# Performance work log

Hardware: AMD Instinct MI355X
Metric: run time of the kernel (lower is better)

Reference implementation:

```python
import jax, jax.numpy as jnp
import numpy as np

K = 10      # neighbors; conv width math 10 -> 3 -> 1
EPS = 1e-5  # InstanceNorm2d default eps (affine=False)
NEG = 0.2   # leaky relu slope


def _instnorm(x):
    m = x.mean(axis=(2, 3), keepdims=True)
    v = x.var(axis=(2, 3), keepdims=True)  # biased var, as in torch instance_norm
    return (x - m) * jax.lax.rsqrt(v + EPS)


def _conv13(x, w, b, s):
    y = jax.lax.conv_general_dilated(x, w, (1, s), 'VALID',
                                     dimension_numbers=('NCHW', 'OIHW', 'NCHW'))
    return y + b[None, :, None, None]


def _block(x, wA, bA, wB, bB):
    # Sequential(conv(1,3,stride(1,3)), IN, ReLU, conv(1,3), IN, ReLU)
    y = jax.nn.relu(_instnorm(_conv13(x, wA, bA, 3)))
    return jax.nn.relu(_instnorm(_conv13(y, wB, bB, 1)))


def _knn_idx(coords, k):
    # coords [B,2,N] -> k nearest neighbor indices [B,N,k] (self excluded)
    pts = coords.transpose(0, 2, 1)
    sq = (pts ** 2).sum(-1)
    dist = sq[:, :, None] + sq[:, None, :] - 2.0 * jnp.einsum('bnc,bmc->bnm', pts, pts)
    dist = jnp.clip(dist, 1e-12)
    _, idx = jax.lax.top_k(-dist, k + 1)  # smallest distances, sorted
    return idx[:, :, 1:]


def _gather_nb(x, idx):
    # x [B,C,N], idx [B,N,k] -> [B,C,N,k]
    return jax.vmap(lambda f, i: f[:, i])(x, idx)


def _graph_feat(feats, idx):
    nb = _gather_nb(feats, idx)
    ctr = jnp.broadcast_to(feats[..., None], nb.shape)
    return jnp.concatenate([ctr, nb - ctr], axis=1)  # [B,2C,N,k]


def _cos_angle(coords, idx):
    nei = _gather_nb(coords, idx)          # [B,2,N,k]
    ctr = coords[..., None]                # [B,2,N,1]
    dot = (ctr * nei).sum(axis=1, keepdims=True)
    na = jnp.sqrt((ctr ** 2).sum(axis=1, keepdims=True))
    nb = jnp.sqrt((nei ** 2).sum(axis=1, keepdims=True))
    return dot / (na * nb)                 # [B,1,N,k]


def _c1(w, x):
    # 1x1 conv, no bias
    return jnp.einsum('oi,bihw->bohw', w, x)


def _forward(coords, features, W1, W2, W3, W3o, a1wA, a1bA, a1wB, a1bB,
             a2wA, a2bA, a2wB, a2bB, angwA, angbA, angwB, angbB):
    B, C, N = features.shape
    lrelu = lambda x: jax.nn.leaky_relu(x, NEG)
    x0 = features[..., None]
    # KNN depends only on coords: all three torch graph builds give identical indices
    idx = _knn_idx(coords, K)
    x1_old = _graph_feat(features, idx)                         # [B,2C,N,K]
    x1 = _block(x1_old, a1wA, a1bA, a1wB, a1bB)                 # [B,C,N,1]
    # angle_enc1 is shared and idx identical -> f_ang1 == f_ang2
    f_ang = _block(_cos_angle(coords, idx), angwA, angbA, angwB, angbB)
    x2 = _block(_graph_feat(x1[..., 0], idx), a2wA, a2bA, a2wB, a2bB)
    x3 = jnp.concatenate([x0, x1 + f_ang, x2 + f_ang], axis=1)  # [B,3C,N,1]
    x3 = lrelu(_instnorm(_c1(W3, x3))).reshape(B, -1, N)
    x1o = lrelu(_instnorm(_c1(W1, x1_old))).max(axis=-1, keepdims=True)   # [B,C,N,1]
    x2o = lrelu(_instnorm(_c1(W2, _graph_feat(x1o[..., 0], idx)))).max(axis=-1, keepdims=True)
    x3o = jnp.concatenate([x0, x1o, x2o], axis=1)               # [B,4C,N,1]
    x3o = lrelu(_instnorm(_c1(W3o, x3o))).reshape(B, -1, N)
    return x3 + x3o


def setup_inputs():
    key = jax.random.key(0)
    ks = jax.random.split(key, 20)
    B, C, N = 4, 128, 4096
    r = lambda i, shp, sc=1.0: jax.random.normal(ks[i], shp, jnp.float32) * sc
    s = 0.05
    return {
        'coords': r(0, (B, 2, N)),
        'features': r(1, (B, C, N)),
        'W1': r(2, (C, 2 * C), s),
        'W2': r(3, (2 * C, 2 * C), s),
        'W3': r(4, (C, 3 * C), s),
        'W3o': r(5, (C, 4 * C), s),
        'a1wA': r(6, (C, 2 * C, 1, 3), s), 'a1bA': r(7, (C,), s),
        'a1wB': r(8, (C, C, 1, 3), s), 'a1bB': r(9, (C,), s),
        'a2wA': r(10, (C, 2 * C, 1, 3), s), 'a2bA': r(11, (C,), s),
        'a2wB': r(12, (C, C, 1, 3), s), 'a2bB': r(13, (C,), s),
        'angwA': r(14, (C, 1, 1, 3), s), 'angbA': r(15, (C,), s),
        'angwB': r(16, (C, C, 1, 3), s), 'angbB': r(17, (C,), s),
    }


def reference(coords, features, W1, W2, W3, W3o, a1wA, a1bA, a1wB, a1bB,
              a2wA, a2bA, a2wB, a2bB, angwA, angbA, angwB, angbB):
    return _forward(coords, features, W1, W2, W3, W3o, a1wA, a1bA, a1wB, a1bB,
                    a2wA, a2bA, a2wB, a2bB, angwA, angbA, angwB, angbB)
```

## Files before the change

### kernel.cpp

```cpp
#include <hip/hip_runtime.h>
#include <hip/hip_bf16.h>

typedef unsigned long long ull;

#define BN 4
#define CH 128
#define NP 4096
#define KNB 10
#define EPSI 1e-5f
#define GM_PTS 16
#define CA_PTS 8

__device__ __forceinline__ ull shfl_xor_u64(ull v, int mask) {
    unsigned lo = (unsigned)(v & 0xFFFFFFFFu);
    unsigned hi = (unsigned)(v >> 32);
    lo = __shfl_xor(lo, mask);
    hi = __shfl_xor(hi, mask);
    return ((ull)hi << 32) | lo;
}

__device__ __forceinline__ int clampj(int j) { return ((unsigned)j < (unsigned)NP) ? j : 0; }

__global__ void pack_convA(const float* __restrict__ w, float* __restrict__ WT) {
    int i = blockIdx.x * 256 + threadIdx.x;
    if (i >= 4 * CH * CH) return;
    int co = i % CH, ci = (i / CH) % CH, s = i / (CH * CH);
    float val;
    if (s == 0) {
        val = 0.f;
        for (int dk = 0; dk < 3; dk++)
            val += w[(co * 256 + ci) * 3 + dk] - w[(co * 256 + 128 + ci) * 3 + dk];
    } else {
        val = w[(co * 256 + 128 + ci) * 3 + (s - 1)];
    }
    WT[i] = val;
}

__global__ void pack_convB(const float* __restrict__ w, float* __restrict__ WT) {
    int i = blockIdx.x * 256 + threadIdx.x;
    if (i >= 3 * CH * CH) return;
    int co = i % CH, ci = (i / CH) % CH, dk = i / (CH * CH);
    WT[i] = w[(co * CH + ci) * 3 + dk];
}

__global__ void pack_uv(const float* __restrict__ w, float* __restrict__ WuT,
                        float* __restrict__ WnT, int Cout) {
    int i = blockIdx.x * 256 + threadIdx.x;
    if (i >= Cout * CH) return;
    int co = i % Cout, ci = i / Cout;
    float a = w[co * 256 + ci], b = w[co * 256 + 128 + ci];
    WuT[i] = a - b;
    WnT[i] = b;
}

__global__ void pack_plain(const float* __restrict__ w, float* __restrict__ WT, int Cin, int Cout) {
    int i = blockIdx.x * 256 + threadIdx.x;
    if (i >= Cin * Cout) return;
    int co = i % Cout, ci = i / Cout;
    WT[i] = w[co * Cin + ci];
}

__global__ void ftrans_kernel(const float* __restrict__ feats, float* __restrict__ F) {
    int i = blockIdx.x * 256 + threadIdx.x;
    if (i >= BN * CH * NP) return;
    int n = i % NP, c = (i / NP) % CH, b = i / (NP * CH);
    F[(b * NP + n) * CH + c] = feats[i];
}

__global__ void knn_kernel(const float* __restrict__ coords, int* __restrict__ IDX) {
    int gw = blockIdx.x * 4 + (threadIdx.x >> 6);
    int b = gw / NP;
    int n = gw % NP;
    int lane = threadIdx.x & 63;
    float xn = coords[(b * 2 + 0) * NP + n];
    float yn = coords[(b * 2 + 1) * NP + n];
    float sn = __fadd_rn(__fmul_rn(xn, xn), __fmul_rn(yn, yn));
    ull a[11];
    #pragma unroll
    for (int q = 0; q < 11; q++) a[q] = 0xFFFFFFFFFFFFFFFFULL;
    for (int m = lane; m < NP; m += 64) {
        float xm = coords[(b * 2 + 0) * NP + m];
        float ym = coords[(b * 2 + 1) * NP + m];
        float sm = __fadd_rn(__fmul_rn(xm, xm), __fmul_rn(ym, ym));
        float dot = __fmaf_rn(yn, ym, __fmul_rn(xn, xm));
        float d = __fsub_rn(__fadd_rn(sn, sm), __fmul_rn(2.0f, dot));
        d = fmaxf(d, 1e-12f);
        ull key = ((ull)__float_as_uint(d) << 32) | (unsigned)m;
        if (key < a[10]) {
            a[10] = key;
            #pragma unroll
            for (int q = 10; q > 0; --q)
                if (a[q] < a[q - 1]) { ull t = a[q]; a[q] = a[q - 1]; a[q - 1] = t; }
        }
    }
    int p = 0;
    for (int r = 0; r < 11; ++r) {
        ull k = (p < 11) ? a[p] : 0xFFFFFFFFFFFFFFFFULL;
        ull mk = k;
        #pragma unroll
        for (int off = 1; off < 64; off <<= 1) {
            ull o = shfl_xor_u64(mk, off);
            mk = (o < mk) ? o : mk;
        }
        if (k == mk) ++p;
        if (lane == 0 && r > 0) IDX[(b * NP + n) * KNB + (r - 1)] = (int)(mk & 0xFFFFFFFFu);
    }
}

__global__ void cosangle_kernel(const float* __restrict__ coords, const int* __restrict__ IDX,
                                float* __restrict__ COSA) {
    int i = blockIdx.x * 256 + threadIdx.x;
    if (i >= BN * NP * KNB) return;
    int n = (i / KNB) % NP, b = i / (KNB * NP);
    int j = clampj(IDX[i]);
    float xc = coords[(b * 2 + 0) * NP + n], yc = coords[(b * 2 + 1) * NP + n];
    float xm = coords[(b * 2 + 0) * NP + j], ym = coords[(b * 2 + 1) * NP + j];
    float dot = xc * xm + yc * ym;
    float na = sqrtf(xc * xc + yc * yc);
    float nb2 = sqrtf(xm * xm + ym * ym);
    COSA[i] = dot / fmaxf(na * nb2, 1e-30f);
}

__global__ __launch_bounds__(256) void convA_kernel(const float* __restrict__ Fin,
                             const int* __restrict__ IDX,
                             const float* __restrict__ WT, float* __restrict__ YA,
                             float* __restrict__ PART) {
    __shared__ float ctr[CA_PTS][CH];
    __shared__ float nb[CA_PTS][9][CH];
    __shared__ int jidx[CA_PTS * 9];
    int b = blockIdx.x / (NP / CA_PTS);
    int chunk = blockIdx.x % (NP / CA_PTS);
    int n0 = chunk * CA_PTS;
    int co = threadIdx.x & 127;
    int half = threadIdx.x >> 7;
    if (threadIdx.x < CA_PTS * 9) {
        int n = threadIdx.x / 9, kk = threadIdx.x % 9;
        jidx[threadIdx.x] = clampj(IDX[(b * NP + n0 + n) * KNB + kk]);
    }
    __syncthreads();
    for (int n = half; n < CA_PTS; n += 2)
        ctr[n][co] = Fin[(b * NP + n0 + n) * CH + co];
    for (int v = half; v < CA_PTS * 9; v += 2)
        nb[v / 9][v % 9][co] = Fin[(b * NP + jidx[v]) * CH + co];
    __syncthreads();
    const int nbase = half * 4;
    float cacc[4] = {0.f, 0.f, 0.f, 0.f};
    for (int ci = 0; ci < CH; ci++) {
        float w = WT[ci * CH + co];
        #pragma unroll
        for (int q = 0; q < 4; q++) cacc[q] += w * ctr[nbase + q][ci];
    }
    float acc[4][3];
    #pragma unroll
    for (int q = 0; q < 4; q++)
        #pragma unroll
        for (int t = 0; t < 3; t++) acc[q][t] = cacc[q];
    for (int dk = 0; dk < 3; dk++) {
        const float* Wd = WT + (1 + dk) * CH * CH;
        for (int ci = 0; ci < CH; ci++) {
            float w = Wd[ci * CH + co];
            #pragma unroll
            for (int q = 0; q < 4; q++)
                #pragma unroll
                for (int t = 0; t < 3; t++)
                    acc[q][t] += w * nb[nbase + q][t * 3 + dk][ci];
        }
    }
    float sum = 0.f, sq = 0.f;
    #pragma unroll
    for (int q = 0; q < 4; q++)
        #pragma unroll
        for (int t = 0; t < 3; t++) {
            float v = acc[q][t];
            YA[((b * NP + n0 + nbase + q) * 3 + t) * CH + co] = v;
            sum += v; sq += v * v;
        }
    int ch2 = chunk * 2 + half;
    PART[((b * (NP / CA_PTS * 2) + ch2) * 256 + co) * 2 + 0] = sum;
    PART[((b * (NP / CA_PTS * 2) + ch2) * 256 + co) * 2 + 1] = sq;
}

__global__ void angA_kernel(const float* __restrict__ COSA, const float* __restrict__ WT,
                            float* __restrict__ YA, float* __restrict__ PART) {
    __shared__ float ca[32][10];
    int b = blockIdx.x / (NP / 32);
    int chunk = blockIdx.x % (NP / 32);
    int n0 = chunk * 32;
    int co = threadIdx.x;
    for (int v = threadIdx.x; v < 320; v += 128) {
        int nn = v / 10, kk = v % 10;
        ca[nn][kk] = COSA[(b * NP + n0 + nn) * KNB + kk];
    }
    float w0 = WT[co], w1 = WT[CH + co], w2 = WT[2 * CH + co];
    __syncthreads();
    float sum = 0.f, sq = 0.f;
    for (int nn = 0; nn < 32; nn++) {
        #pragma unroll
        for (int t = 0; t < 3; t++) {
            float v = w0 * ca[nn][3 * t] + w1 * ca[nn][3 * t + 1] + w2 * ca[nn][3 * t + 2];
            YA[((b * NP + n0 + nn) * 3 + t) * CH + co] = v;
            sum += v; sq += v * v;
        }
    }
    PART[((b * (NP / 32) + chunk) * 256 + co) * 2 + 0] = sum;
    PART[((b * (NP / 32) + chunk) * 256 + co) * 2 + 1] = sq;
}

__global__ void pixel_gemm(const float* __restrict__ IN_, const float* __restrict__ WT,
                           float* __restrict__ OUT, int Cin, int Cout,
                           const float* __restrict__ STATS, int slot,
                           float* __restrict__ PART) {
    extern __shared__ float ldsin[];
    int b = blockIdx.x / (NP / 8);
    int chunk = blockIdx.x % (NP / 8);
    int n0 = chunk * 8;
    int co = threadIdx.x;
    if (slot >= 0) {
        for (int v = threadIdx.x; v < 8 * Cin; v += blockDim.x) {
            int c = v & 127;
            float m = STATS[((slot * BN + b) * 256 + c) * 2 + 0];
            float r = STATS[((slot * BN + b) * 256 + c) * 2 + 1];
            float x = (IN_[(size_t)(b * NP + n0) * Cin + v] - m) * r;
            ldsin[v] = fmaxf(x, 0.f);
        }
    } else {
        for (int v = threadIdx.x; v < 8 * Cin; v += blockDim.x)
            ldsin[v] = IN_[(size_t)(b * NP + n0) * Cin + v];
    }
    __syncthreads();
    float acc[8] = {0.f, 0.f, 0.f, 0.f, 0.f, 0.f, 0.f, 0.f};
    for (int ci = 0; ci < Cin; ci++) {
        float w = WT[ci * Cout + co];
        #pragma unroll
        for (int nn = 0; nn < 8; nn++) acc[nn] += w * ldsin[nn * Cin + ci];
    }
    float sum = 0.f, sq = 0.f;
    #pragma unroll
    for (int nn = 0; nn < 8; nn++) {
        OUT[(size_t)(b * NP + n0 + nn) * Cout + co] = acc[nn];
        sum += acc[nn]; sq += acc[nn] * acc[nn];
    }
    if (PART) {
        PART[((b * (NP / 8) + chunk) * 256 + co) * 2 + 0] = sum;
        PART[((b * (NP / 8) + chunk) * 256 + co) * 2 + 1] = sq;
    }
}

__global__ void stats_final(const float* __restrict__ PART, float* __restrict__ STATS,
                            int S, int Cc, int slot, int nch) {
    __shared__ float ssum[256], ssq[256];
    int bc = blockIdx.x;
    int b = bc / Cc, c = bc % Cc;
    float sum = 0.f, sq = 0.f;
    for (int ch = threadIdx.x; ch < nch; ch += 256) {
        sum += PART[((b * nch + ch) * 256 + c) * 2 + 0];
        sq  += PART[((b * nch + ch) * 256 + c) * 2 + 1];
    }
    ssum[threadIdx.x] = sum; ssq[threadIdx.x] = sq;
    __syncthreads();
    for (int s = 128; s > 0; s >>= 1) {
        if (threadIdx.x < s) {
            ssum[threadIdx.x] += ssum[threadIdx.x + s];
            ssq[threadIdx.x]  += ssq[threadIdx.x + s];
        }
        __syncthreads();
    }
    if (threadIdx.x == 0) {
        float mean = ssum[0] / (float)S;
        float var = fmaxf(ssq[0] / (float)S - mean * mean, 0.f);
        STATS[((slot * BN + b) * 256 + c) * 2 + 0] = mean;
        STATS[((slot * BN + b) * 256 + c) * 2 + 1] = rsqrtf(var + EPSI);
    }
}

__global__ void norm_act(float* __restrict__ X, const float* __restrict__ STATS,
                         int S, int Cc, int slot, int act) {
    int i = blockIdx.x * 256 + threadIdx.x;
    if (i >= BN * S * Cc) return;
    int c = i % Cc;
    int b = i / (S * Cc);
    float m = STATS[((slot * BN + b) * 256 + c) * 2 + 0];
    float r = STATS[((slot * BN + b) * 256 + c) * 2 + 1];
    float v = (X[i] - m) * r;
    if (act == 0) v = fmaxf(v, 0.f);
    else v = (v >= 0.f) ? v : 0.2f * v;
    X[i] = v;
}

__global__ void gathermax_fused(const float* __restrict__ X, const float* __restrict__ Wu,
                                const float* __restrict__ V, const int* __restrict__ IDX,
                                float* __restrict__ M, float* __restrict__ PART, int Cout) {
    __shared__ float rows[GM_PTS * CH];
    int b = blockIdx.x / (NP / GM_PTS);
    int chunk = blockIdx.x % (NP / GM_PTS);
    int n0 = chunk * GM_PTS;
    int c = threadIdx.x;
    for (int v = threadIdx.x; v < GM_PTS * CH; v += blockDim.x)
        rows[v] = X[(size_t)(b * NP + n0) * CH + v];
    __syncthreads();
    float acc[GM_PTS];
    #pragma unroll
    for (int nn = 0; nn < GM_PTS; nn++) acc[nn] = 0.f;
    for (int ci = 0; ci < CH; ci++) {
        float w = Wu[ci * Cout + c];
        #pragma unroll
        for (int nn = 0; nn < GM_PTS; nn++) acc[nn] += w * rows[nn * CH + ci];
    }
    float sum = 0.f, sq = 0.f;
    for (int nn = 0; nn < GM_PTS; nn++) {
        float u = acc[nn];
        float best = -3.4e38f;
        for (int k = 0; k < KNB; k++) {
            int j = clampj(IDX[(b * NP + n0 + nn) * KNB + k]);
            float v = u + V[(size_t)(b * NP + j) * Cout + c];
            sum += v; sq += v * v;
            best = fmaxf(best, v);
        }
        M[(size_t)(b * NP + n0 + nn) * Cout + c] = best;
    }
    PART[((b * (NP / GM_PTS) + chunk) * 256 + c) * 2 + 0] = sum;
    PART[((b * (NP / GM_PTS) + chunk) * 256 + c) * 2 + 1] = sq;
}

__global__ void head3_kernel(const float* __restrict__ F, const float* __restrict__ X1,
                             const float* __restrict__ X2, const float* __restrict__ FANG,
                             const float* __restrict__ WT, float* __restrict__ Y3,
                             float* __restrict__ PART) {
    __shared__ float lds[8 * 384];
    int b = blockIdx.x / (NP / 8);
    int chunk = blockIdx.x % (NP / 8);
    int n0 = chunk * 8;
    int co = threadIdx.x;
    for (int v = threadIdx.x; v < 8 * 384; v += 128) {
        int nn = v / 384, q = v % 384;
        int part = q / 128, ci = q % 128;
        size_t base = (size_t)(b * NP + n0 + nn) * CH + ci;
        float val;
        if (part == 0) val = F[base];
        else if (part == 1) val = X1[base] + FANG[base];
        else val = X2[base] + FANG[base];
        lds[v] = val;
    }
    __syncthreads();
    float acc[8] = {0.f, 0.f, 0.f, 0.f, 0.f, 0.f, 0.f, 0.f};
    for (int ci = 0; ci < 384; ci++) {
        float w = WT[ci * CH + co];
        #pragma unroll
        for (int nn = 0; nn < 8; nn++) acc[nn] += w * lds[nn * 384 + ci];
    }
    float sum = 0.f, sq = 0.f;
    #pragma unroll
    for (int nn = 0; nn < 8; nn++) {
        Y3[(size_t)(b * NP + n0 + nn) * CH + co] = acc[nn];
        sum += acc[nn]; sq += acc[nn] * acc[nn];
    }
    PART[((b * (NP / 8) + chunk) * 256 + co) * 2 + 0] = sum;
    PART[((b * (NP / 8) + chunk) * 256 + co) * 2 + 1] = sq;
}

__global__ void head3o_kernel(const float* __restrict__ F, const float* __restrict__ X1O,
                              const float* __restrict__ X2O, const float* __restrict__ WT,
                              float* __restrict__ Y3O, float* __restrict__ PART) {
    __shared__ float lds[8 * 512];
    int b = blockIdx.x / (NP / 8);
    int chunk = blockIdx.x % (NP / 8);
    int n0 = chunk * 8;
    int co = threadIdx.x;
    for (int v = threadIdx.x; v < 8 * 512; v += 128) {
        int nn = v / 512, q = v % 512;
        float val;
        if (q < 128) val = F[(size_t)(b * NP + n0 + nn) * CH + q];
        else if (q < 256) val = X1O[(size_t)(b * NP + n0 + nn) * CH + (q - 128)];
        else val = X2O[(size_t)(b * NP + n0 + nn) * 256 + (q - 256)];
        lds[v] = val;
    }
    __syncthreads();
    float acc[8] = {0.f, 0.f, 0.f, 0.f, 0.f, 0.f, 0.f, 0.f};
    for (int ci = 0; ci < 512; ci++) {
        float w = WT[ci * CH + co];
        #pragma unroll
        for (int nn = 0; nn < 8; nn++) acc[nn] += w * lds[nn * 512 + ci];
    }
    float sum = 0.f, sq = 0.f;
    #pragma unroll
    for (int nn = 0; nn < 8; nn++) {
        Y3O[(size_t)(b * NP + n0 + nn) * CH + co] = acc[nn];
        sum += acc[nn]; sq += acc[nn] * acc[nn];
    }
    PART[((b * (NP / 8) + chunk) * 256 + co) * 2 + 0] = sum;
    PART[((b * (NP / 8) + chunk) * 256 + co) * 2 + 1] = sq;
}

__global__ void final_kernel(const float* __restrict__ Y3, const float* __restrict__ Y3O,
                             const float* __restrict__ STATS, float* __restrict__ out) {
    __shared__ float T[64][129];
    int b = blockIdx.x / (NP / 64);
    int n0 = (blockIdx.x % (NP / 64)) * 64;
    int co = threadIdx.x;
    float m3 = STATS[((8 * BN + b) * 256 + co) * 2 + 0];
    float r3 = STATS[((8 * BN + b) * 256 + co) * 2 + 1];
    float m3o = STATS[((9 * BN + b) * 256 + co) * 2 + 0];
    float r3o = STATS[((9 * BN + b) * 256 + co) * 2 + 1];
    for (int j = 0; j < 64; j++) {
        size_t idx = (size_t)(b * NP + n0 + j) * CH + co;
        float v3 = (Y3[idx] - m3) * r3;
        v3 = (v3 >= 0.f) ? v3 : 0.2f * v3;
        float v3o = (Y3O[idx] - m3o) * r3o;
        v3o = (v3o >= 0.f) ? v3o : 0.2f * v3o;
        T[j][co] = v3 + v3o;
    }
    __syncthreads();
    for (int rr = 0; rr < 64; rr++) {
        int r = rr * 2 + (threadIdx.x >> 6);
        int j = threadIdx.x & 63;
        out[(size_t)(b * CH + r) * NP + n0 + j] = T[j][r];
    }
}

extern "C" void kernel_launch(void* const* d_in, const int* in_sizes, int n_in,
                              void* d_out, int out_size, void* d_ws, size_t ws_size,
                              hipStream_t stream) {
    const float* coords   = (const float*)d_in[0];
    const float* features = (const float*)d_in[1];
    const float* W1   = (const float*)d_in[2];
    const float* W2   = (const float*)d_in[3];
    const float* W3   = (const float*)d_in[4];
    const float* W3o  = (const float*)d_in[5];
    const float* a1wA = (const float*)d_in[6];
    const float* a1wB = (const float*)d_in[8];
    const float* a2wA = (const float*)d_in[10];
    const float* a2wB = (const float*)d_in[12];
    const float* angwA = (const float*)d_in[14];
    const float* angwB = (const float*)d_in[16];
    float* out = (float*)d_out;
    float* ws = (float*)d_ws;
    (void)ws_size; (void)in_sizes; (void)n_in; (void)out_size;

    size_t off = 0;
    float* WA1T  = ws + off; off += 4 * CH * CH;
    float* WA2T  = ws + off; off += 4 * CH * CH;
    float* WB1T  = ws + off; off += 3 * CH * CH;
    float* WB2T  = ws + off; off += 3 * CH * CH;
    float* WBAT  = ws + off; off += 3 * CH * CH;
    float* WANGA = ws + off; off += 512;
    float* W1U   = ws + off; off += CH * CH;
    float* W1N   = ws + off; off += CH * CH;
    float* W2U   = ws + off; off += CH * 256;
    float* W2N   = ws + off; off += CH * 256;
    float* W3T   = ws + off; off += 384 * CH;
    float* W3OT  = ws + off; off += 512 * CH;
    int*   IDX   = (int*)(ws + off); off += (size_t)BN * NP * KNB;
    float* COSA  = ws + off; off += (size_t)BN * NP * KNB;
    float* PART  = ws + off; off += (size_t)BN * 1024 * 256 * 2;
    float* STATS = ws + off; off += 10 * BN * 256 * 2;
    const size_t UNIT = (size_t)BN * NP * CH;
    float* POOL  = ws + off; off += 7 * UNIT;

    float* F    = POOL + 0 * UNIT;
    float* YA   = POOL + 1 * UNIT;
    float* X1   = POOL + 4 * UNIT;
    float* FANG = POOL + 5 * UNIT;
    float* X2   = POOL + 6 * UNIT;
    float* Y3   = POOL + 1 * UNIT;
    float* V1   = POOL + 2 * UNIT;
    float* M1   = POOL + 6 * UNIT;
    float* V2   = POOL + 4 * UNIT;
    float* M2   = POOL + 2 * UNIT;
    float* Y3O  = POOL + 4 * UNIT;

    pack_convA<<<(4 * CH * CH + 255) / 256, 256, 0, stream>>>(a1wA, WA1T);
    pack_convA<<<(4 * CH * CH + 255) / 256, 256, 0, stream>>>(a2wA, WA2T);
    pack_convB<<<(3 * CH * CH + 255) / 256, 256, 0, stream>>>(a1wB, WB1T);
    pack_convB<<<(3 * CH * CH + 255) / 256, 256, 0, stream>>>(a2wB, WB2T);
    pack_convB<<<(3 * CH * CH + 255) / 256, 256, 0, stream>>>(angwB, WBAT);
    pack_uv<<<(CH * CH + 255) / 256, 256, 0, stream>>>(W1, W1U, W1N, CH);
    pack_uv<<<(CH * 256 + 255) / 256, 256, 0, stream>>>(W2, W2U, W2N, 256);
    pack_plain<<<(384 * CH + 255) / 256, 256, 0, stream>>>(W3, W3T, 384, CH);
    pack_plain<<<(512 * CH + 255) / 256, 256, 0, stream>>>(W3o, W3OT, 512, CH);
    pack_plain<<<(3 * CH + 255) / 256, 256, 0, stream>>>(angwA, WANGA, 3, CH);

    ftrans_kernel<<<(BN * CH * NP + 255) / 256, 256, 0, stream>>>(features, F);
    knn_kernel<<<BN * NP / 4, 256, 0, stream>>>(coords, IDX);
    cosangle_kernel<<<(BN * NP * KNB + 255) / 256, 256, 0, stream>>>(coords, IDX, COSA);

    auto sfin = [&](int S, int Cc, int slot, int nch) {
        stats_final<<<BN * Cc, 256, 0, stream>>>(PART, STATS, S, Cc, slot, nch);
    };
    auto norm = [&](float* X, int S, int Cc, int slot, int act) {
        int tot = BN * S * Cc;
        norm_act<<<(tot + 255) / 256, 256, 0, stream>>>(X, STATS, S, Cc, slot, act);
    };

    convA_kernel<<<BN * (NP / CA_PTS), 256, 0, stream>>>(F, IDX, WA1T, YA, PART);
    sfin(3 * NP, CH, 0, NP / CA_PTS * 2);
    pixel_gemm<<<BN * (NP / 8), 128, 8 * 384 * 4, stream>>>(YA, WB1T, X1, 384, CH, STATS, 0, PART);
    sfin(NP, CH, 1, NP / 8);
    norm(X1, NP, CH, 1, 0);

    angA_kernel<<<BN * (NP / 32), 128, 0, stream>>>(COSA, WANGA, YA, PART);
    sfin(3 * NP, CH, 2, NP / 32);
    pixel_gemm<<<BN * (NP / 8), 128, 8 * 384 * 4, stream>>>(YA, WBAT, FANG, 384, CH, STATS, 2, PART);
    sfin(NP, CH, 3, NP / 8);
    norm(FANG, NP, CH, 3, 0);

    convA_kernel<<<BN * (NP / CA_PTS), 256, 0, stream>>>(X1, IDX, WA2T, YA, PART);
    sfin(3 * NP, CH, 4, NP / CA_PTS * 2);
    pixel_gemm<<<BN * (NP / 8), 128, 8 * 384 * 4, stream>>>(YA, WB2T, X2, 384, CH, STATS, 4, PART);
    sfin(NP, CH, 5, NP / 8);
    norm(X2, NP, CH, 5, 0);

    head3_kernel<<<BN * (NP / 8), 128, 0, stream>>>(F, X1, X2, FANG, W3T, Y3, PART);
    sfin(NP, CH, 8, NP / 8);

    pixel_gemm<<<BN * (NP / 8), 128, 8 * 128 * 4, stream>>>(F, W1N, V1, 128, CH, STATS, -1, nullptr);
    gathermax_fused<<<BN * (NP / GM_PTS), CH, 0, stream>>>(F, W1U, V1, IDX, M1, PART, CH);
    sfin(NP * KNB, CH, 6, NP / GM_PTS);
    norm(M1, NP, CH, 6, 1);

    pixel_gemm<<<BN * (NP / 8), 256, 8 * 128 * 4, stream>>>(M1, W2N, V2, 128, 256, STATS, -1, nullptr);
    gathermax_fused<<<BN * (NP / GM_PTS), 256, 0, stream>>>(M1, W2U, V2, IDX, M2, PART, 256);
    sfin(NP * KNB, 256, 7, NP / GM_PTS);
    norm(M2, NP, 256, 7, 1);

    head3o_kernel<<<BN * (NP / 8), 128, 0, stream>>>(F, M1, M2, W3OT, Y3O, PART);
    sfin(NP, CH, 9, NP / 8);
    final_kernel<<<BN * (NP / 64), 128, 0, stream>>>(Y3, Y3O, STATS, out);
}
```

Before: 1.048 ms.

## Register-tile all pointwise GEMMs with float4 output channels and vectorized loads

```diff
diff --git a/kernel.cpp b/kernel.cpp
--- a/kernel.cpp
+++ b/kernel.cpp
@@ -11,6 +11,9 @@
 #define GM_PTS 16
 #define CA_PTS 8
 
+#define FMA4(A, W, F) do { (A).x += (W).x*(F); (A).y += (W).y*(F); \
+                           (A).z += (W).z*(F); (A).w += (W).w*(F); } while(0)
+
 __device__ __forceinline__ ull shfl_xor_u64(ull v, int mask) {
     unsigned lo = (unsigned)(v & 0xFFFFFFFFu);
     unsigned hi = (unsigned)(v >> 32);
@@ -21,9 +24,7 @@
 
 __device__ __forceinline__ int clampj(int j) { return ((unsigned)j < (unsigned)NP) ? j : 0; }
 
-__global__ void pack_convA(const float* __restrict__ w, float* __restrict__ WT) {
-    int i = blockIdx.x * 256 + threadIdx.x;
-    if (i >= 4 * CH * CH) return;
+__device__ __forceinline__ void d_packA(const float* w, float* WT, int i) {
     int co = i % CH, ci = (i / CH) % CH, s = i / (CH * CH);
     float val;
     if (s == 0) {
@@ -35,29 +36,45 @@
     }
     WT[i] = val;
 }
-
-__global__ void pack_convB(const float* __restrict__ w, float* __restrict__ WT) {
-    int i = blockIdx.x * 256 + threadIdx.x;
-    if (i >= 3 * CH * CH) return;
+__device__ __forceinline__ void d_packB(const float* w, float* WT, int i) {
     int co = i % CH, ci = (i / CH) % CH, dk = i / (CH * CH);
     WT[i] = w[(co * CH + ci) * 3 + dk];
 }
-
-__global__ void pack_uv(const float* __restrict__ w, float* __restrict__ WuT,
-                        float* __restrict__ WnT, int Cout) {
-    int i = blockIdx.x * 256 + threadIdx.x;
-    if (i >= Cout * CH) return;
+__device__ __forceinline__ void d_packUV(const float* w, float* Wu, float* Wn, int Cout, int i) {
     int co = i % Cout, ci = i / Cout;
-    float a = w[co * 256 + ci], b = w[co * 256 + 128 + ci];
-    WuT[i] = a - b;
-    WnT[i] = b;
-}
-
-__global__ void pack_plain(const float* __restrict__ w, float* __restrict__ WT, int Cin, int Cout) {
-    int i = blockIdx.x * 256 + threadIdx.x;
-    if (i >= Cin * Cout) return;
+    float a = w[co * 256 + ci], bb = w[co * 256 + 128 + ci];
+    Wu[i] = a - bb; Wn[i] = bb;
+}
+__device__ __forceinline__ void d_packP(const float* w, float* WT, int Cin, int Cout, int i) {
     int co = i % Cout, ci = i / Cout;
     WT[i] = w[co * Cin + ci];
+}
+
+__global__ void pack_all(const float* __restrict__ a1wA, const float* __restrict__ a2wA,
+                         const float* __restrict__ a1wB, const float* __restrict__ a2wB,
+                         const float* __restrict__ angwB, const float* __restrict__ W1,
+                         const float* __restrict__ W2, const float* __restrict__ W3,
+                         const float* __restrict__ W3o, const float* __restrict__ angwA,
+                         float* __restrict__ WA1T, float* __restrict__ WA2T,
+                         float* __restrict__ WB1T, float* __restrict__ WB2T,
+                         float* __restrict__ WBAT,
+                         float* __restrict__ W1U, float* __restrict__ W1N,
+                         float* __restrict__ W2U, float* __restrict__ W2N,
+                         float* __restrict__ W3T, float* __restrict__ W3OT,
+                         float* __restrict__ WANGA) {
+    int i = blockIdx.x * 256 + threadIdx.x;
+    const int sA = 4 * CH * CH;
+    const int sB = 3 * CH * CH;
+    if (i < sA) { d_packA(a1wA, WA1T, i); return; } i -= sA;
+    if (i < sA) { d_packA(a2wA, WA2T, i); return; } i -= sA;
+    if (i < sB) { d_packB(a1wB, WB1T, i); return; } i -= sB;
+    if (i < sB) { d_packB(a2wB, WB2T, i); return; } i -= sB;
+    if (i < sB) { d_packB(angwB, WBAT, i); return; } i -= sB;
+    if (i < CH * CH) { d_packUV(W1, W1U, W1N, CH, i); return; } i -= CH * CH;
+    if (i < CH * 256) { d_packUV(W2, W2U, W2N, 256, i); return; } i -= CH * 256;
+    if (i < 384 * CH) { d_packP(W3, W3T, 384, CH, i); return; } i -= 384 * CH;
+    if (i < 512 * CH) { d_packP(W3o, W3OT, 512, CH, i); return; } i -= 512 * CH;
+    if (i < 3 * CH) { d_packP(angwA, WANGA, 3, CH, i); return; }
 }
 
 __global__ void ftrans_kernel(const float* __restrict__ feats, float* __restrict__ F) {
@@ -125,59 +142,95 @@
                              const int* __restrict__ IDX,
                              const float* __restrict__ WT, float* __restrict__ YA,
                              float* __restrict__ PART) {
-    __shared__ float ctr[CA_PTS][CH];
-    __shared__ float nb[CA_PTS][9][CH];
+    __shared__ __align__(16) float ctr[CA_PTS][CH];
+    __shared__ __align__(16) float nb[CA_PTS][9][CH];
     __shared__ int jidx[CA_PTS * 9];
     int b = blockIdx.x / (NP / CA_PTS);
     int chunk = blockIdx.x % (NP / CA_PTS);
     int n0 = chunk * CA_PTS;
-    int co = threadIdx.x & 127;
-    int half = threadIdx.x >> 7;
+    int cog = threadIdx.x & 31;
+    int pg  = threadIdx.x >> 5;
     if (threadIdx.x < CA_PTS * 9) {
         int n = threadIdx.x / 9, kk = threadIdx.x % 9;
         jidx[threadIdx.x] = clampj(IDX[(b * NP + n0 + n) * KNB + kk]);
     }
     __syncthreads();
-    for (int n = half; n < CA_PTS; n += 2)
-        ctr[n][co] = Fin[(b * NP + n0 + n) * CH + co];
-    for (int v = half; v < CA_PTS * 9; v += 2)
-        nb[v / 9][v % 9][co] = Fin[(b * NP + jidx[v]) * CH + co];
-    __syncthreads();
-    const int nbase = half * 4;
-    float cacc[4] = {0.f, 0.f, 0.f, 0.f};
-    for (int ci = 0; ci < CH; ci++) {
-        float w = WT[ci * CH + co];
+    {
+        int v4 = threadIdx.x;
+        int n = v4 >> 5, c4 = v4 & 31;
+        *(float4*)&ctr[n][c4 * 4] =
+            *(const float4*)&Fin[(size_t)(b * NP + n0 + n) * CH + c4 * 4];
+    }
+    for (int v4 = threadIdx.x; v4 < CA_PTS * 9 * 32; v4 += 256) {
+        int n = v4 / 288, rem = v4 % 288, kk = rem >> 5, c4 = rem & 31;
+        *(float4*)&nb[n][kk][c4 * 4] =
+            *(const float4*)&Fin[(size_t)(b * NP + jidx[n * 9 + kk]) * CH + c4 * 4];
+    }
+    __syncthreads();
+    const float4* W4 = (const float4*)WT;
+    float4 cacc; cacc.x = cacc.y = cacc.z = cacc.w = 0.f;
+    {
+        const float* xb = &ctr[pg][0];
+        for (int ci = 0; ci < CH; ci += 4) {
+            float4 x = *(const float4*)&xb[ci];
+            #pragma unroll
+            for (int u = 0; u < 4; ++u) {
+                float4 w = W4[(ci + u) * 32 + cog];
+                float f = ((const float*)&x)[u];
+                FMA4(cacc, w, f);
+            }
+        }
+    }
+    float4 t0 = cacc, t1 = cacc, t2 = cacc;
+    for (int dk = 0; dk < 3; ++dk) {
+        const float4* Wd = W4 + (size_t)(1 + dk) * (CH * 32);
+        const float* b0 = &nb[pg][0 * 3 + dk][0];
+        const float* b1 = &nb[pg][1 * 3 + dk][0];
+        const float* b2 = &nb[pg][2 * 3 + dk][0];
+        for (int ci = 0; ci < CH; ci += 4) {
+            float4 x0 = *(const float4*)&b0[ci];
+            float4 x1 = *(const float4*)&b1[ci];
+            float4 x2 = *(const float4*)&b2[ci];
+            #pragma unroll
+            for (int u = 0; u < 4; ++u) {
+                float4 w = Wd[(ci + u) * 32 + cog];
+                float f0 = ((const float*)&x0)[u];
+                float f1 = ((const float*)&x1)[u];
+                float f2 = ((const float*)&x2)[u];
+                FMA4(t0, w, f0); FMA4(t1, w, f1); FMA4(t2, w, f2);
+            }
+        }
+    }
+    {
+        size_t base = ((size_t)(b * NP + n0 + pg) * 3) * CH + cog * 4;
+        *(float4*)&YA[base + 0 * CH] = t0;
+        *(float4*)&YA[base + 1 * CH] = t1;
+        *(float4*)&YA[base + 2 * CH] = t2;
+    }
+    float s4[4], q4[4];
+    s4[0] = t0.x + t1.x + t2.x; q4[0] = t0.x*t0.x + t1.x*t1.x + t2.x*t2.x;
+    s4[1] = t0.y + t1.y + t2.y; q4[1] = t0.y*t0.y + t1.y*t1.y + t2.y*t2.y;
+    s4[2] = t0.z + t1.z + t2.z; q4[2] = t0.z*t0.z + t1.z*t1.z + t2.z*t2.z;
+    s4[3] = t0.w + t1.w + t2.w; q4[3] = t0.w*t0.w + t1.w*t1.w + t2.w*t2.w;
+    __syncthreads();
+    float* red = &nb[0][0][0];
+    #pragma unroll
+    for (int j = 0; j < 4; ++j) {
+        red[((pg * 32 + cog) * 4 + j) * 2 + 0] = s4[j];
+        red[((pg * 32 + cog) * 4 + j) * 2 + 1] = q4[j];
+    }
+    __syncthreads();
+    if (threadIdx.x < CH) {
+        int c = threadIdx.x;
+        float ss = 0.f, qq = 0.f;
         #pragma unroll
-        for (int q = 0; q < 4; q++) cacc[q] += w * ctr[nbase + q][ci];
-    }
-    float acc[4][3];
-    #pragma unroll
-    for (int q = 0; q < 4; q++)
-        #pragma unroll
-        for (int t = 0; t < 3; t++) acc[q][t] = cacc[q];
-    for (int dk = 0; dk < 3; dk++) {
-        const float* Wd = WT + (1 + dk) * CH * CH;
-        for (int ci = 0; ci < CH; ci++) {
-            float w = Wd[ci * CH + co];
-            #pragma unroll
-            for (int q = 0; q < 4; q++)
-                #pragma unroll
-                for (int t = 0; t < 3; t++)
-                    acc[q][t] += w * nb[nbase + q][t * 3 + dk][ci];
-        }
-    }
-    float sum = 0.f, sq = 0.f;
-    #pragma unroll
-    for (int q = 0; q < 4; q++)
-        #pragma unroll
-        for (int t = 0; t < 3; t++) {
-            float v = acc[q][t];
-            YA[((b * NP + n0 + nbase + q) * 3 + t) * CH + co] = v;
-            sum += v; sq += v * v;
-        }
-    int ch2 = chunk * 2 + half;
-    PART[((b * (NP / CA_PTS * 2) + ch2) * 256 + co) * 2 + 0] = sum;
-    PART[((b * (NP / CA_PTS * 2) + ch2) * 256 + co) * 2 + 1] = sq;
+        for (int g = 0; g < 8; ++g) {
+            ss += red[((g * 32 + (c >> 2)) * 4 + (c & 3)) * 2 + 0];
+            qq += red[((g * 32 + (c >> 2)) * 4 + (c & 3)) * 2 + 1];
+        }
+        PART[((size_t)(b * (NP / CA_PTS) + chunk) * 256 + c) * 2 + 0] = ss;
+        PART[((size_t)(b * (NP / CA_PTS) + chunk) * 256 + c) * 2 + 1] = qq;
+    }
 }
 
 __global__ void angA_kernel(const float* __restrict__ COSA, const float* __restrict__ WT,
@@ -206,44 +259,109 @@
     PART[((b * (NP / 32) + chunk) * 256 + co) * 2 + 1] = sq;
 }
 
-__global__ void pixel_gemm(const float* __restrict__ IN_, const float* __restrict__ WT,
-                           float* __restrict__ OUT, int Cin, int Cout,
-                           const float* __restrict__ STATS, int slot,
-                           float* __restrict__ PART) {
-    extern __shared__ float ldsin[];
-    int b = blockIdx.x / (NP / 8);
-    int chunk = blockIdx.x % (NP / 8);
-    int n0 = chunk * 8;
-    int co = threadIdx.x;
+template <int CIN, int NCOG>
+__device__ __forceinline__ void gemm_16pt(const float* lds, const float* __restrict__ WT,
+                                          int cog, int pg, float4 acc[4]) {
+    const float4* W4 = (const float4*)WT;
+    const float* xb = lds + pg * 4 * CIN;
+    for (int ci = 0; ci < CIN; ci += 4) {
+        float4 x0 = *(const float4*)&xb[0 * CIN + ci];
+        float4 x1 = *(const float4*)&xb[1 * CIN + ci];
+        float4 x2 = *(const float4*)&xb[2 * CIN + ci];
+        float4 x3 = *(const float4*)&xb[3 * CIN + ci];
+        #pragma unroll
+        for (int u = 0; u < 4; ++u) {
+            float4 w = W4[(ci + u) * NCOG + cog];
+            float f0 = ((const float*)&x0)[u];
+            float f1 = ((const float*)&x1)[u];
+            float f2 = ((const float*)&x2)[u];
+            float f3 = ((const float*)&x3)[u];
+            FMA4(acc[0], w, f0); FMA4(acc[1], w, f1);
+            FMA4(acc[2], w, f2); FMA4(acc[3], w, f3);
+        }
+    }
+}
+
+template <int NCOG>
+__device__ __forceinline__ void reduce_stats(const float* s4, const float* q4,
+                                             float* red, float* __restrict__ PART,
+                                             int b, int chunk, int nchunks,
+                                             int pg, int cog) {
+    constexpr int COUT = NCOG * 4;
+    __syncthreads();
+    #pragma unroll
+    for (int j = 0; j < 4; ++j) {
+        red[((pg * NCOG + cog) * 4 + j) * 2 + 0] = s4[j];
+        red[((pg * NCOG + cog) * 4 + j) * 2 + 1] = q4[j];
+    }
+    __syncthreads();
+    int c = threadIdx.x;
+    if (c < COUT) {
+        float ss = 0.f, qq = 0.f;
+        #pragma unroll
+        for (int g = 0; g < 4; ++g) {
+            ss += red[((g * NCOG + (c >> 2)) * 4 + (c & 3)) * 2 + 0];
+            qq += red[((g * NCOG + (c >> 2)) * 4 + (c & 3)) * 2 + 1];
+        }
+        PART[((size_t)(b * nchunks + chunk) * 256 + c) * 2 + 0] = ss;
+        PART[((size_t)(b * nchunks + chunk) * 256 + c) * 2 + 1] = qq;
+    }
+}
+
+template <int NCOG>
+__device__ __forceinline__ void out16(const float4 acc[4], float* __restrict__ OUT,
+                                      int b, int n0, int pg, int cog,
+                                      float s4[4], float q4[4]) {
+    constexpr int COUT = NCOG * 4;
+    #pragma unroll
+    for (int p = 0; p < 4; ++p) {
+        *(float4*)&OUT[(size_t)(b * NP + n0 + pg * 4 + p) * COUT + cog * 4] = acc[p];
+        s4[0] += acc[p].x; s4[1] += acc[p].y; s4[2] += acc[p].z; s4[3] += acc[p].w;
+        q4[0] += acc[p].x * acc[p].x; q4[1] += acc[p].y * acc[p].y;
+        q4[2] += acc[p].z * acc[p].z; q4[3] += acc[p].w * acc[p].w;
+    }
+}
+
+template <int CIN, int NCOG>
+__global__ void pixel_gemm_t(const float* __restrict__ IN_, const float* __restrict__ WT,
+                             float* __restrict__ OUT, const float* __restrict__ STATS,
+                             int slot, float* __restrict__ PART) {
+    constexpr int COUT = NCOG * 4;
+    constexpr int BD = 4 * NCOG;
+    __shared__ __align__(16) float ldsin[16 * CIN];
+    int b = blockIdx.x / (NP / 16);
+    int chunk = blockIdx.x % (NP / 16);
+    int n0 = chunk * 16;
+    int cog = threadIdx.x & (NCOG - 1);
+    int pg = threadIdx.x / NCOG;
+    constexpr int nv4 = 16 * CIN / 4;
     if (slot >= 0) {
-        for (int v = threadIdx.x; v < 8 * Cin; v += blockDim.x) {
-            int c = v & 127;
-            float m = STATS[((slot * BN + b) * 256 + c) * 2 + 0];
-            float r = STATS[((slot * BN + b) * 256 + c) * 2 + 1];
-            float x = (IN_[(size_t)(b * NP + n0) * Cin + v] - m) * r;
-            ldsin[v] = fmaxf(x, 0.f);
+        int cbase = (4 * threadIdx.x) & 127;
+        const float* st = &STATS[((slot * BN + b) * 256 + cbase) * 2];
+        float m0 = st[0], r0 = st[1], m1 = st[2], r1 = st[3];
+        float m2 = st[4], r2 = st[5], m3 = st[6], r3 = st[7];
+        for (int v4 = threadIdx.x; v4 < nv4; v4 += BD) {
+            float4 x = *(const float4*)&IN_[(size_t)(b * NP + n0) * CIN + 4 * v4];
+            x.x = fmaxf((x.x - m0) * r0, 0.f);
+            x.y = fmaxf((x.y - m1) * r1, 0.f);
+            x.z = fmaxf((x.z - m2) * r2, 0.f);
+            x.w = fmaxf((x.w - m3) * r3, 0.f);
+            *(float4*)&ldsin[4 * v4] = x;
         }
     } else {
-        for (int v = threadIdx.x; v < 8 * Cin; v += blockDim.x)
-            ldsin[v] = IN_[(size_t)(b * NP + n0) * Cin + v];
-    }
-    __syncthreads();
-    float acc[8] = {0.f, 0.f, 0.f, 0.f, 0.f, 0.f, 0.f, 0.f};
-    for (int ci = 0; ci < Cin; ci++) {
-        float w = WT[ci * Cout + co];
-        #pragma unroll
-        for (int nn = 0; nn < 8; nn++) acc[nn] += w * ldsin[nn * Cin + ci];
-    }
-    float sum = 0.f, sq = 0.f;
-    #pragma unroll
-    for (int nn = 0; nn < 8; nn++) {
-        OUT[(size_t)(b * NP + n0 + nn) * Cout + co] = acc[nn];
-        sum += acc[nn]; sq += acc[nn] * acc[nn];
-    }
-    if (PART) {
-        PART[((b * (NP / 8) + chunk) * 256 + co) * 2 + 0] = sum;
-        PART[((b * (NP / 8) + chunk) * 256 + co) * 2 + 1] = sq;
-    }
+        for (int v4 = threadIdx.x; v4 < nv4; v4 += BD)
+            *(float4*)&ldsin[4 * v4] =
+                *(const float4*)&IN_[(size_t)(b * NP + n0) * CIN + 4 * v4];
+    }
+    __syncthreads();
+    float4 acc[4];
+    #pragma unroll
+    for (int p = 0; p < 4; ++p) acc[p].x = acc[p].y = acc[p].z = acc[p].w = 0.f;
+    gemm_16pt<CIN, NCOG>(ldsin, WT, cog, pg, acc);
+    float s4[4] = {0,0,0,0}, q4[4] = {0,0,0,0};
+    out16<NCOG>(acc, OUT, b, n0, pg, cog, s4, q4);
+    if (PART)
+        reduce_stats<NCOG>(s4, q4, ldsin, PART, b, chunk, NP / 16, pg, cog);
 }
 
 __global__ void stats_final(const float* __restrict__ PART, float* __restrict__ STATS,
@@ -287,108 +405,109 @@
     X[i] = v;
 }
 
-__global__ void gathermax_fused(const float* __restrict__ X, const float* __restrict__ Wu,
-                                const float* __restrict__ V, const int* __restrict__ IDX,
-                                float* __restrict__ M, float* __restrict__ PART, int Cout) {
-    __shared__ float rows[GM_PTS * CH];
+template <int NCOG>
+__global__ void gathermax_t(const float* __restrict__ X, const float* __restrict__ Wu,
+                            const float* __restrict__ V, const int* __restrict__ IDX,
+                            float* __restrict__ M, float* __restrict__ PART) {
+    constexpr int COUT = NCOG * 4;
+    __shared__ __align__(16) float rows[GM_PTS * CH];
     int b = blockIdx.x / (NP / GM_PTS);
     int chunk = blockIdx.x % (NP / GM_PTS);
     int n0 = chunk * GM_PTS;
-    int c = threadIdx.x;
-    for (int v = threadIdx.x; v < GM_PTS * CH; v += blockDim.x)
-        rows[v] = X[(size_t)(b * NP + n0) * CH + v];
-    __syncthreads();
-    float acc[GM_PTS];
-    #pragma unroll
-    for (int nn = 0; nn < GM_PTS; nn++) acc[nn] = 0.f;
-    for (int ci = 0; ci < CH; ci++) {
-        float w = Wu[ci * Cout + c];
-        #pragma unroll
-        for (int nn = 0; nn < GM_PTS; nn++) acc[nn] += w * rows[nn * CH + ci];
-    }
-    float sum = 0.f, sq = 0.f;
-    for (int nn = 0; nn < GM_PTS; nn++) {
-        float u = acc[nn];
-        float best = -3.4e38f;
-        for (int k = 0; k < KNB; k++) {
-            int j = clampj(IDX[(b * NP + n0 + nn) * KNB + k]);
-            float v = u + V[(size_t)(b * NP + j) * Cout + c];
-            sum += v; sq += v * v;
-            best = fmaxf(best, v);
-        }
-        M[(size_t)(b * NP + n0 + nn) * Cout + c] = best;
-    }
-    PART[((b * (NP / GM_PTS) + chunk) * 256 + c) * 2 + 0] = sum;
-    PART[((b * (NP / GM_PTS) + chunk) * 256 + c) * 2 + 1] = sq;
+    int cog = threadIdx.x & (NCOG - 1);
+    int pg = threadIdx.x / NCOG;
+    for (int v4 = threadIdx.x; v4 < GM_PTS * CH / 4; v4 += COUT)
+        *(float4*)&rows[v4 * 4] = *(const float4*)&X[(size_t)(b * NP + n0) * CH + v4 * 4];
+    __syncthreads();
+    float4 acc[4];
+    #pragma unroll
+    for (int p = 0; p < 4; ++p) acc[p].x = acc[p].y = acc[p].z = acc[p].w = 0.f;
+    gemm_16pt<CH, NCOG>(rows, Wu, cog, pg, acc);
+    float s4[4] = {0,0,0,0}, q4[4] = {0,0,0,0};
+    #pragma unroll
+    for (int p = 0; p < 4; ++p) {
+        int nn = n0 + pg * 4 + p;
+        float4 u = acc[p];
+        float4 best; best.x = best.y = best.z = best.w = -3.4e38f;
+        for (int k = 0; k < KNB; ++k) {
+            int j = clampj(IDX[(b * NP + nn) * KNB + k]);
+            float4 vv = *(const float4*)&V[(size_t)(b * NP + j) * COUT + cog * 4];
+            vv.x += u.x; vv.y += u.y; vv.z += u.z; vv.w += u.w;
+            s4[0] += vv.x; s4[1] += vv.y; s4[2] += vv.z; s4[3] += vv.w;
+            q4[0] += vv.x * vv.x; q4[1] += vv.y * vv.y;
+            q4[2] += vv.z * vv.z; q4[3] += vv.w * vv.w;
+            best.x = fmaxf(best.x, vv.x); best.y = fmaxf(best.y, vv.y);
+            best.z = fmaxf(best.z, vv.z); best.w = fmaxf(best.w, vv.w);
+        }
+        *(float4*)&M[(size_t)(b * NP + nn) * COUT + cog * 4] = best;
+    }
+    __syncthreads();
+    reduce_stats<NCOG>(s4, q4, rows, PART, b, chunk, NP / GM_PTS, pg, cog);
 }
 
 __global__ void head3_kernel(const float* __restrict__ F, const float* __restrict__ X1,
                              const float* __restrict__ X2, const float* __restrict__ FANG,
                              const float* __restrict__ WT, float* __restrict__ Y3,
                              float* __restrict__ PART) {
-    __shared__ float lds[8 * 384];
-    int b = blockIdx.x / (NP / 8);
-    int chunk = blockIdx.x % (NP / 8);
-    int n0 = chunk * 8;
-    int co = threadIdx.x;
-    for (int v = threadIdx.x; v < 8 * 384; v += 128) {
-        int nn = v / 384, q = v % 384;
-        int part = q / 128, ci = q % 128;
-        size_t base = (size_t)(b * NP + n0 + nn) * CH + ci;
-        float val;
-        if (part == 0) val = F[base];
-        else if (part == 1) val = X1[base] + FANG[base];
-        else val = X2[base] + FANG[base];
-        lds[v] = val;
-    }
-    __syncthreads();
-    float acc[8] = {0.f, 0.f, 0.f, 0.f, 0.f, 0.f, 0.f, 0.f};
-    for (int ci = 0; ci < 384; ci++) {
-        float w = WT[ci * CH + co];
-        #pragma unroll
-        for (int nn = 0; nn < 8; nn++) acc[nn] += w * lds[nn * 384 + ci];
-    }
-    float sum = 0.f, sq = 0.f;
-    #pragma unroll
-    for (int nn = 0; nn < 8; nn++) {
-        Y3[(size_t)(b * NP + n0 + nn) * CH + co] = acc[nn];
-        sum += acc[nn]; sq += acc[nn] * acc[nn];
-    }
-    PART[((b * (NP / 8) + chunk) * 256 + co) * 2 + 0] = sum;
-    PART[((b * (NP / 8) + chunk) * 256 + co) * 2 + 1] = sq;
+    __shared__ __align__(16) float lds[16 * 384];
+    int b = blockIdx.x / (NP / 16);
+    int chunk = blockIdx.x % (NP / 16);
+    int n0 = chunk * 16;
+    int cog = threadIdx.x & 31;
+    int pg = threadIdx.x >> 5;
+    for (int v4 = threadIdx.x; v4 < 16 * 96; v4 += 128) {
+        int nn = v4 / 96, q4 = v4 % 96;
+        int part = q4 >> 5, c4 = q4 & 31;
+        size_t base = (size_t)(b * NP + n0 + nn) * CH + c4 * 4;
+        float4 val;
+        if (part == 0) val = *(const float4*)&F[base];
+        else {
+            const float* src = (part == 1) ? X1 : X2;
+            float4 xx = *(const float4*)&src[base];
+            float4 aa = *(const float4*)&FANG[base];
+            val.x = xx.x + aa.x; val.y = xx.y + aa.y;
+            val.z = xx.z + aa.z; val.w = xx.w + aa.w;
+        }
+        *(float4*)&lds[v4 * 4] = val;
+    }
+    __syncthreads();
+    float4 acc[4];
+    #pragma unroll
+    for (int p = 0; p < 4; ++p) acc[p].x = acc[p].y = acc[p].z = acc[p].w = 0.f;
+    gemm_16pt<384, 32>(lds, WT, cog, pg, acc);
+    float s4[4] = {0,0,0,0}, q4[4] = {0,0,0,0};
+    out16<32>(acc, Y3, b, n0, pg, cog, s4, q4);
+    reduce_stats<32>(s4, q4, lds, PART, b, chunk, NP / 16, pg, cog);
 }
 
 __global__ void head3o_kernel(const float* __restrict__ F, const float* __restrict__ X1O,
                               const float* __restrict__ X2O, const float* __restrict__ WT,
                               float* __restrict__ Y3O, float* __restrict__ PART) {
-    __shared__ float lds[8 * 512];
-    int b = blockIdx.x / (NP / 8);
-    int chunk = blockIdx.x % (NP / 8);
-    int n0 = chunk * 8;
-    int co = threadIdx.x;
-    for (int v = threadIdx.x; v < 8 * 512; v += 128) {
-        int nn = v / 512, q = v % 512;
-        float val;
-        if (q < 128) val = F[(size_t)(b * NP + n0 + nn) * CH + q];
-        else if (q < 256) val = X1O[(size_t)(b * NP + n0 + nn) * CH + (q - 128)];
-        else val = X2O[(size_t)(b * NP + n0 + nn) * 256 + (q - 256)];
-        lds[v] = val;
-    }
-    __syncthreads();
-    float acc[8] = {0.f, 0.f, 0.f, 0.f, 0.f, 0.f, 0.f, 0.f};
-    for (int ci = 0; ci < 512; ci++) {
-        float w = WT[ci * CH + co];
-        #pragma unroll
-        for (int nn = 0; nn < 8; nn++) acc[nn] += w * lds[nn * 512 + ci];
-    }
-    float sum = 0.f, sq = 0.f;
-    #pragma unroll
-    for (int nn = 0; nn < 8; nn++) {
-        Y3O[(size_t)(b * NP + n0 + nn) * CH + co] = acc[nn];
-        sum += acc[nn]; sq += acc[nn] * acc[nn];
-    }
-    PART[((b * (NP / 8) + chunk) * 256 + co) * 2 + 0] = sum;
-    PART[((b * (NP / 8) + chunk) * 256 + co) * 2 + 1] = sq;
+    __shared__ __align__(16) float lds[16 * 512];
+    int b = blockIdx.x / (NP / 16);
+    int chunk = blockIdx.x % (NP / 16);
+    int n0 = chunk * 16;
+    int cog = threadIdx.x & 31;
+    int pg = threadIdx.x >> 5;
+    for (int v4 = threadIdx.x; v4 < 16 * 128; v4 += 128) {
+        int nn = v4 >> 7, q4 = v4 & 127;
+        float4 val;
+        if (q4 < 32)
+            val = *(const float4*)&F[(size_t)(b * NP + n0 + nn) * CH + q4 * 4];
+        else if (q4 < 64)
+            val = *(const float4*)&X1O[(size_t)(b * NP + n0 + nn) * CH + (q4 - 32) * 4];
+        else
+            val = *(const float4*)&X2O[(size_t)(b * NP + n0 + nn) * 256 + (q4 - 64) * 4];
+        *(float4*)&lds[v4 * 4] = val;
+    }
+    __syncthreads();
+    float4 acc[4];
+    #pragma unroll
+    for (int p = 0; p < 4; ++p) acc[p].x = acc[p].y = acc[p].z = acc[p].w = 0.f;
+    gemm_16pt<512, 32>(lds, WT, cog, pg, acc);
+    float s4[4] = {0,0,0,0}, q4[4] = {0,0,0,0};
+    out16<32>(acc, Y3O, b, n0, pg, cog, s4, q4);
+    reduce_stats<32>(s4, q4, lds, PART, b, chunk, NP / 16, pg, cog);
 }
 
 __global__ void final_kernel(const float* __restrict__ Y3, const float* __restrict__ Y3O,
@@ -468,16 +587,9 @@
     float* M2   = POOL + 2 * UNIT;
     float* Y3O  = POOL + 4 * UNIT;
 
-    pack_convA<<<(4 * CH * CH + 255) / 256, 256, 0, stream>>>(a1wA, WA1T);
-    pack_convA<<<(4 * CH * CH + 255) / 256, 256, 0, stream>>>(a2wA, WA2T);
-    pack_convB<<<(3 * CH * CH + 255) / 256, 256, 0, stream>>>(a1wB, WB1T);
-    pack_convB<<<(3 * CH * CH + 255) / 256, 256, 0, stream>>>(a2wB, WB2T);
-    pack_convB<<<(3 * CH * CH + 255) / 256, 256, 0, stream>>>(angwB, WBAT);
-    pack_uv<<<(CH * CH + 255) / 256, 256, 0, stream>>>(W1, W1U, W1N, CH);
-    pack_uv<<<(CH * 256 + 255) / 256, 256, 0, stream>>>(W2, W2U, W2N, 256);
-    pack_plain<<<(384 * CH + 255) / 256, 256, 0, stream>>>(W3, W3T, 384, CH);
-    pack_plain<<<(512 * CH + 255) / 256, 256, 0, stream>>>(W3o, W3OT, 512, CH);
-    pack_plain<<<(3 * CH + 255) / 256, 256, 0, stream>>>(angwA, WANGA, 3, CH);
+    pack_all<<<1730, 256, 0, stream>>>(a1wA, a2wA, a1wB, a2wB, angwB, W1, W2, W3, W3o, angwA,
+                                       WA1T, WA2T, WB1T, WB2T, WBAT,
+                                       W1U, W1N, W2U, W2N, W3T, W3OT, WANGA);
 
     ftrans_kernel<<<(BN * CH * NP + 255) / 256, 256, 0, stream>>>(features, F);
     knn_kernel<<<BN * NP / 4, 256, 0, stream>>>(coords, IDX);
@@ -492,37 +604,37 @@
     };
 
     convA_kernel<<<BN * (NP / CA_PTS), 256, 0, stream>>>(F, IDX, WA1T, YA, PART);
-    sfin(3 * NP, CH, 0, NP / CA_PTS * 2);
-    pixel_gemm<<<BN * (NP / 8), 128, 8 * 384 * 4, stream>>>(YA, WB1T, X1, 384, CH, STATS, 0, PART);
-    sfin(NP, CH, 1, NP / 8);
+    sfin(3 * NP, CH, 0, NP / CA_PTS);
+    pixel_gemm_t<384, 32><<<BN * (NP / 16), 128, 0, stream>>>(YA, WB1T, X1, STATS, 0, PART);
+    sfin(NP, CH, 1, NP / 16);
     norm(X1, NP, CH, 1, 0);
 
     angA_kernel<<<BN * (NP / 32), 128, 0, stream>>>(COSA, WANGA, YA, PART);
     sfin(3 * NP, CH, 2, NP / 32);
-    pixel_gemm<<<BN * (NP / 8), 128, 8 * 384 * 4, stream>>>(YA, WBAT, FANG, 384, CH, STATS, 2, PART);
-    sfin(NP, CH, 3, NP / 8);
+    pixel_gemm_t<384, 32><<<BN * (NP / 16), 128, 0, stream>>>(YA, WBAT, FANG, STATS, 2, PART);
+    sfin(NP, CH, 3, NP / 16);
     norm(FANG, NP, CH, 3, 0);
 
     convA_kernel<<<BN * (NP / CA_PTS), 256, 0, stream>>>(X1, IDX, WA2T, YA, PART);
-    sfin(3 * NP, CH, 4, NP / CA_PTS * 2);
-    pixel_gemm<<<BN * (NP / 8), 128, 8 * 384 * 4, stream>>>(YA, WB2T, X2, 384, CH, STATS, 4, PART);
-    sfin(NP, CH, 5, NP / 8);
+    sfin(3 * NP, CH, 4, NP / CA_PTS);
+    pixel_gemm_t<384, 32><<<BN * (NP / 16), 128, 0, stream>>>(YA, WB2T, X2, STATS, 4, PART);
+    sfin(NP, CH, 5, NP / 16);
     norm(X2, NP, CH, 5, 0);
 
-    head3_kernel<<<BN * (NP / 8), 128, 0, stream>>>(F, X1, X2, FANG, W3T, Y3, PART);
-    sfin(NP, CH, 8, NP / 8);
-
-    pixel_gemm<<<BN * (NP / 8), 128, 8 * 128 * 4, stream>>>(F, W1N, V1, 128, CH, STATS, -1, nullptr);
-    gathermax_fused<<<BN * (NP / GM_PTS), CH, 0, stream>>>(F, W1U, V1, IDX, M1, PART, CH);
+    head3_kernel<<<BN * (NP / 16), 128, 0, stream>>>(F, X1, X2, FANG, W3T, Y3, PART);
+    sfin(NP, CH, 8, NP / 16);
+
+    pixel_gemm_t<128, 32><<<BN * (NP / 16), 128, 0, stream>>>(F, W1N, V1, STATS, -1, nullptr);
+    gathermax_t<32><<<BN * (NP / GM_PTS), 128, 0, stream>>>(F, W1U, V1, IDX, M1, PART);
     sfin(NP * KNB, CH, 6, NP / GM_PTS);
     norm(M1, NP, CH, 6, 1);
 
-    pixel_gemm<<<BN * (NP / 8), 256, 8 * 128 * 4, stream>>>(M1, W2N, V2, 128, 256, STATS, -1, nullptr);
-    gathermax_fused<<<BN * (NP / GM_PTS), 256, 0, stream>>>(M1, W2U, V2, IDX, M2, PART, 256);
+    pixel_gemm_t<128, 64><<<BN * (NP / 16), 256, 0, stream>>>(M1, W2N, V2, STATS, -1, nullptr);
+    gathermax_t<64><<<BN * (NP / GM_PTS), 256, 0, stream>>>(M1, W2U, V2, IDX, M2, PART);
     sfin(NP * KNB, 256, 7, NP / GM_PTS);
     norm(M2, NP, 256, 7, 1);
 
-    head3o_kernel<<<BN * (NP / 8), 128, 0, stream>>>(F, M1, M2, W3OT, Y3O, PART);
-    sfin(NP, CH, 9, NP / 8);
+    head3o_kernel<<<BN * (NP / 16), 128, 0, stream>>>(F, M1, M2, W3OT, Y3O, PART);
+    sfin(NP, CH, 9, NP / 16);
     final_kernel<<<BN * (NP / 64), 128, 0, stream>>>(Y3, Y3O, STATS, out);
 }
```

Result: faster. 927.4 us (-11.5%).
